# Optimization experiments

Measured on AMD Instinct MI355X. Metric: run time of the kernel, lower is better.

## Reference

```python
import jax, jax.numpy as jnp
import numpy as np

N_NODES = 100000
N_EDGES = 1600000
IN_DIM, H_DIM, OUT_DIM = 256, 128, 2
NEG_SLOPE = 0.2  # PyG GATConv default


def gat_conv(x, edge_index, W, a_src, a_dst, b):
    """Single-head PyG GATConv (heads=1, concat, add_self_loops=True)."""
    n = x.shape[0]
    loops = jnp.arange(n, dtype=edge_index.dtype)
    src = jnp.concatenate([edge_index[0], loops])  # [E+N]
    dst = jnp.concatenate([edge_index[1], loops])
    h = x @ W                                      # [N, F_out]
    # attention logits per edge: LeakyReLU(a_src.h_src + a_dst.h_dst)
    e = jax.nn.leaky_relu((h @ a_src)[src] + (h @ a_dst)[dst], NEG_SLOPE)
    # segment softmax over incoming edges of each destination node
    m = jax.ops.segment_max(e, dst, num_segments=n)
    ex = jnp.exp(e - m[dst])
    denom = jax.ops.segment_sum(ex, dst, num_segments=n)
    alpha = ex / denom[dst]                        # self-loops guarantee denom > 0
    # scatter-aggregate weighted messages
    out = jax.ops.segment_sum(h[src] * alpha[:, None], dst, num_segments=n)
    return out + b


def setup_inputs() -> dict:
    key = jax.random.key(0)
    ks = jax.random.split(key, 10)
    glorot = lambda k, shape: jax.random.normal(k, shape, dtype=jnp.float32) * jnp.sqrt(
        2.0 / (shape[0] + shape[-1])
    ).astype(jnp.float32)
    return {
        "x": jax.random.normal(ks[0], (N_NODES, IN_DIM), dtype=jnp.float32),
        "edge_index": jax.random.randint(ks[1], (2, N_EDGES), 0, N_NODES, dtype=jnp.int64 if jax.config.jax_enable_x64 else jnp.int32),
        "W1": glorot(ks[2], (IN_DIM, H_DIM)),
        "a1_src": glorot(ks[3], (H_DIM,)),
        "a1_dst": glorot(ks[4], (H_DIM,)),
        "b1": jnp.zeros((H_DIM,), dtype=jnp.float32),
        "W2": glorot(ks[5], (H_DIM, OUT_DIM)),
        "a2_src": glorot(ks[6], (OUT_DIM,)),
        "a2_dst": glorot(ks[7], (OUT_DIM,)),
        "b2": jnp.zeros((OUT_DIM,), dtype=jnp.float32),
    }


def reference(x, edge_index, W1, a1_src, a1_dst, b1, W2, a2_src, a2_dst, b2):
    h1 = jax.nn.relu(gat_conv(x, edge_index, W1, a1_src, a1_dst, b1))
    # F.dropout(p=0.5) is identity in eval mode
    return gat_conv(h1, edge_index, W2, a2_src, a2_dst, b2)
```

## Files before the change

### kernel.cpp

```cpp
#include <hip/hip_runtime.h>
#include <hip/hip_bf16.h>

#define N_NODES 100000
#define IN_DIM 256
#define H_DIM 128
#define NEG_SLOPE 0.2f

#define NBUCK 391
#define BKT_CAP 8192
#define P1_EPT 16

__device__ __forceinline__ float lrelu(float v) { return v > 0.f ? v : NEG_SLOPE * v; }
__device__ __forceinline__ float bflo(unsigned u) { return __uint_as_float(u << 16); }
__device__ __forceinline__ float bfhi(unsigned u) { return __uint_as_float(u & 0xffff0000u); }
__device__ __forceinline__ unsigned short f2bf(float f) {
    unsigned u = __float_as_uint(f);
    return (unsigned short)((u + 0x7fffu + ((u >> 16) & 1u)) >> 16);
}
__device__ __forceinline__ float rdlanef(float v, int j) {
    return __uint_as_float(__builtin_amdgcn_readlane(__float_as_uint(v), j));
}

typedef short bfrag __attribute__((ext_vector_type(8)));
typedef float f32x4 __attribute__((ext_vector_type(4)));

__global__ __launch_bounds__(512) void fused_gemm_bin1(const float* __restrict__ x,
                                                       const float* __restrict__ W,
                                                       const float* __restrict__ a_src,
                                                       const float* __restrict__ a_dst,
                                                       unsigned short* __restrict__ hb,
                                                       float* __restrict__ as1,
                                                       float* __restrict__ ad1,
                                                       const int* __restrict__ src,
                                                       const int* __restrict__ dst,
                                                       int* __restrict__ bktAlloc,
                                                       unsigned long long* __restrict__ tmp,
                                                       int E, int p1B) {
    __shared__ __align__(16) char smemraw[65536];
    const int tid = threadIdx.x;

    if ((int)blockIdx.x < p1B) {
        int* hist  = (int*)smemraw;
        int* basev = hist + 512;
        int* hist2 = basev + 512;
        hist[tid] = 0; hist2[tid] = 0;
        __syncthreads();
        const int e0 = blockIdx.x * (512 * P1_EPT) + tid * P1_EPT;
        int sv[P1_EPT], dv[P1_EPT];
#pragma unroll
        for (int i = 0; i < P1_EPT; ++i) {
            int e = e0 + i;
            if (e < E) { sv[i] = src[e]; dv[i] = dst[e]; }
            else dv[i] = -1;
        }
#pragma unroll
        for (int i = 0; i < P1_EPT; ++i)
            if (dv[i] >= 0) atomicAdd(&hist[dv[i] >> 8], 1);
        __syncthreads();
        {
            int c = hist[tid];
            basev[tid] = c ? atomicAdd(&bktAlloc[tid], c) : 0;
        }
        __syncthreads();
#pragma unroll
        for (int i = 0; i < P1_EPT; ++i) {
            if (dv[i] >= 0) {
                int b = dv[i] >> 8;
                int r = atomicAdd(&hist2[b], 1);
                int pos = basev[b] + r;
                if (pos < BKT_CAP)
                    tmp[(size_t)b * BKT_CAP + pos] =
                        ((unsigned long long)(unsigned)dv[i] << 32) | (unsigned)sv[i];
            }
        }
        return;
    }

    unsigned short* lds = (unsigned short*)smemraw;
    const int w = tid >> 6;
    const int lane = tid & 63;
    const int lo = lane & 15;
    const int hi = lane >> 4;
    const int row0 = ((int)blockIdx.x - p1B) * 128;

    {
        int col = tid & 127;
        int kb = tid >> 7;
        int c7 = col & 7;
#pragma unroll
        for (int i = 0; i < 16; ++i) {
            int k0 = i * 16 + kb * 4;
            float w0 = W[(k0 + 0) * H_DIM + col];
            float w1 = W[(k0 + 1) * H_DIM + col];
            float w2 = W[(k0 + 2) * H_DIM + col];
            float w3 = W[(k0 + 3) * H_DIM + col];
            int kblk = k0 >> 3;
            int rem = k0 & 7;
            unsigned short* d = &lds[col * 256 + ((kblk ^ c7) << 3) + rem];
            d[0] = f2bf(w0); d[1] = f2bf(w1); d[2] = f2bf(w2); d[3] = f2bf(w3);
        }
    }
    __syncthreads();

    int arow = row0 + w * 16 + lo;
    if (arow >= N_NODES) arow = N_NODES - 1;
    const float* xrow = x + (size_t)arow * IN_DIM + hi * 8;

    f32x4 acc[8] = {};
#pragma unroll
    for (int kc = 0; kc < 8; ++kc) {
        float4 xa = *reinterpret_cast<const float4*>(xrow + kc * 32);
        float4 xb = *reinterpret_cast<const float4*>(xrow + kc * 32 + 4);
        bfrag a;
        a[0] = (short)f2bf(xa.x); a[1] = (short)f2bf(xa.y);
        a[2] = (short)f2bf(xa.z); a[3] = (short)f2bf(xa.w);
        a[4] = (short)f2bf(xb.x); a[5] = (short)f2bf(xb.y);
        a[6] = (short)f2bf(xb.z); a[7] = (short)f2bf(xb.w);
        int kblk = kc * 4 + hi;
#pragma unroll
        for (int c = 0; c < 8; ++c) {
            int col = c * 16 + lo;
            const bfrag b = *reinterpret_cast<const bfrag*>(
                &lds[col * 256 + ((kblk ^ (col & 7)) << 3)]);
            acc[c] = __builtin_amdgcn_mfma_f32_16x16x32_bf16(a, b, acc[c], 0, 0, 0);
        }
    }

    float asv[8], adv[8];
#pragma unroll
    for (int c = 0; c < 8; ++c) { asv[c] = a_src[c * 16 + lo]; adv[c] = a_dst[c * 16 + lo]; }
#pragma unroll
    for (int q = 0; q < 4; ++q) {
        float ps = 0.f, pd = 0.f;
#pragma unroll
        for (int c = 0; c < 8; ++c) { ps += acc[c][q] * asv[c]; pd += acc[c][q] * adv[c]; }
#pragma unroll
        for (int off = 8; off; off >>= 1) {
            ps += __shfl_xor(ps, off);
            pd += __shfl_xor(pd, off);
        }
        int grow = row0 + w * 16 + hi * 4 + q;
        if (lo == 0 && grow < N_NODES) { as1[grow] = ps; ad1[grow] = pd; }
    }

    __syncthreads();
#pragma unroll
    for (int c = 0; c < 8; ++c)
#pragma unroll
        for (int q = 0; q < 4; ++q)
            lds[(w * 16 + hi * 4 + q) * 128 + c * 16 + lo] = f2bf(acc[c][q]);
    __syncthreads();
#pragma unroll
    for (int i = 0; i < 4; ++i) {
        int idx = i * 512 + tid;
        int row = idx >> 4;
        int chunk = idx & 15;
        int grow = row0 + row;
        if (grow < N_NODES) {
            uint4 v = *reinterpret_cast<const uint4*>(&lds[row * 128 + chunk * 8]);
            *reinterpret_cast<uint4*>(&hb[(size_t)grow * H_DIM + chunk * 8]) = v;
        }
    }
}

__global__ __launch_bounds__(512) void bin_pass2(const unsigned long long* __restrict__ tmp,
                                                 const int* __restrict__ bktAlloc,
                                                 int* __restrict__ rowptr,
                                                 int* __restrict__ col) {
    __shared__ int bscan[512];
    __shared__ int cnt[256], sc[256], rp[256];
    __shared__ int s_ebeg;
    const int b = blockIdx.x;
    const int nb0 = b << 8;
    const int nmax = min(256, N_NODES - nb0);
    const int tid = threadIdx.x;

    int v = (tid < NBUCK) ? min(bktAlloc[tid], BKT_CAP) : 0;
    bscan[tid] = v;
    __syncthreads();
    for (int off = 1; off < 512; off <<= 1) {
        int u = (tid >= off) ? bscan[tid - off] : 0;
        __syncthreads();
        bscan[tid] += u;
        __syncthreads();
    }
    const int myCnt = min(bktAlloc[b], BKT_CAP);
    if (tid == 0) s_ebeg = bscan[b] - myCnt;
    if (tid < 256) cnt[tid] = 0;
    __syncthreads();
    const int ebeg = s_ebeg;
    const unsigned long long* btmp = tmp + (size_t)b * BKT_CAP;

    for (int i = tid; i < myCnt; i += 512)
        atomicAdd(&cnt[(int)(unsigned)(btmp[i] >> 32) - nb0], 1);
    __syncthreads();
    if (tid < 256) sc[tid] = cnt[tid];
    __syncthreads();
    for (int off = 1; off < 256; off <<= 1) {
        int u = (tid < 256 && tid >= off) ? sc[tid - off] : 0;
        __syncthreads();
        if (tid < 256) sc[tid] += u;
        __syncthreads();
    }
    if (tid < 256) { rp[tid] = ebeg + sc[tid] - cnt[tid]; cnt[tid] = 0; }
    __syncthreads();
    if (tid < nmax) rowptr[nb0 + tid] = rp[tid];
    if (b == NBUCK - 1 && tid == 0) rowptr[N_NODES] = ebeg + myCnt;
    for (int i = tid; i < myCnt; i += 512) {
        unsigned long long e = btmp[i];
        int s = (int)(unsigned)e;
        int dl = (int)(unsigned)(e >> 32) - nb0;
        int off = atomicAdd(&cnt[dl], 1);
        col[rp[dl] + off] = s;
    }
}

__global__ __launch_bounds__(256) void agg1_kernel(const unsigned int* __restrict__ hbu,
                                                   const float* __restrict__ as1,
                                                   const float* __restrict__ ad1,
                                                   const int* __restrict__ rowptr,
                                                   const int* __restrict__ col,
                                                   const float* __restrict__ b1,
                                                   const float* __restrict__ W2,
                                                   const float* __restrict__ a2s,
                                                   const float* __restrict__ a2d,
                                                   float* __restrict__ h2,
                                                   float* __restrict__ as2,
                                                   float* __restrict__ ad2) {
    int node = blockIdx.x * 4 + (threadIdx.x >> 6);
    int lane = threadIdx.x & 63;
    if (node >= N_NODES) return;

    float adi = ad1[node];
    float wself = __expf(lrelu(as1[node] + adi));
    unsigned hvs = hbu[(unsigned)node * 64u + lane];
    float ax = wself * bflo(hvs), ay = wself * bfhi(hvs);
    float lsum = 0.0f;

    const int beg = rowptr[node], end = rowptr[node + 1];
    for (int p0 = beg; p0 < end; p0 += 64) {
        const int jn = min(64, end - p0);
        int idx = p0 + (lane < jn ? lane : 0);
        int s_l = col[idx];
        float e_l = (lane < jn) ? __expf(lrelu(as1[s_l] + adi)) : 0.0f;
        lsum += e_l;
        int j = 0;
        for (; j + 8 <= jn; j += 8) {
            const unsigned* r0 = hbu + ((size_t)__builtin_amdgcn_readlane(s_l, j)     << 6);
            const unsigned* r1 = hbu + ((size_t)__builtin_amdgcn_readlane(s_l, j + 1) << 6);
            const unsigned* r2 = hbu + ((size_t)__builtin_amdgcn_readlane(s_l, j + 2) << 6);
            const unsigned* r3 = hbu + ((size_t)__builtin_amdgcn_readlane(s_l, j + 3) << 6);
            const unsigned* r4 = hbu + ((size_t)__builtin_amdgcn_readlane(s_l, j + 4) << 6);
            const unsigned* r5 = hbu + ((size_t)__builtin_amdgcn_readlane(s_l, j + 5) << 6);
            const unsigned* r6 = hbu + ((size_t)__builtin_amdgcn_readlane(s_l, j + 6) << 6);
            const unsigned* r7 = hbu + ((size_t)__builtin_amdgcn_readlane(s_l, j + 7) << 6);
            unsigned v0 = r0[lane];
            unsigned v1 = r1[lane];
            unsigned v2 = r2[lane];
            unsigned v3 = r3[lane];
            unsigned v4 = r4[lane];
            unsigned v5 = r5[lane];
            unsigned v6 = r6[lane];
            unsigned v7 = r7[lane];
            float w0 = rdlanef(e_l, j);
            float w1 = rdlanef(e_l, j + 1);
            float w2 = rdlanef(e_l, j + 2);
            float w3 = rdlanef(e_l, j + 3);
            float w4 = rdlanef(e_l, j + 4);
            float w5 = rdlanef(e_l, j + 5);
            float w6 = rdlanef(e_l, j + 6);
            float w7 = rdlanef(e_l, j + 7);
            ax += (w0 * bflo(v0) + w1 * bflo(v1)) + (w2 * bflo(v2) + w3 * bflo(v3))
                + (w4 * bflo(v4) + w5 * bflo(v5)) + (w6 * bflo(v6) + w7 * bflo(v7));
            ay += (w0 * bfhi(v0) + w1 * bfhi(v1)) + (w2 * bfhi(v2) + w3 * bfhi(v3))
                + (w4 * bfhi(v4) + w5 * bfhi(v5)) + (w6 * bfhi(v6) + w7 * bfhi(v7));
        }
        for (; j < jn; ++j) {
            const unsigned* r = hbu + ((size_t)__builtin_amdgcn_readlane(s_l, j) << 6);
            float w = rdlanef(e_l, j);
            unsigned v = r[lane];
            ax += w * bflo(v);
            ay += w * bfhi(v);
        }
    }
#pragma unroll
    for (int off = 32; off; off >>= 1) lsum += __shfl_xor(lsum, off);
    float inv = 1.0f / (lsum + wself);

    float2 bb = *reinterpret_cast<const float2*>(&b1[lane * 2]);
    float o0 = fmaxf(ax * inv + bb.x, 0.0f);
    float o1 = fmaxf(ay * inv + bb.y, 0.0f);

    float4 w2 = *reinterpret_cast<const float4*>(&W2[lane * 4]);
    float p0 = o0 * w2.x + o1 * w2.z;
    float p1 = o0 * w2.y + o1 * w2.w;
#pragma unroll
    for (int off = 32; off; off >>= 1) {
        p0 += __shfl_xor(p0, off);
        p1 += __shfl_xor(p1, off);
    }
    if (lane == 0) {
        h2[node * 2 + 0] = p0;
        h2[node * 2 + 1] = p1;
        as2[node] = p0 * a2s[0] + p1 * a2s[1];
        ad2[node] = p0 * a2d[0] + p1 * a2d[1];
    }
}

__global__ __launch_bounds__(256) void agg2_kernel(const float* __restrict__ h2,
                                                   const float* __restrict__ as2,
                                                   const float* __restrict__ ad2,
                                                   const int* __restrict__ rowptr,
                                                   const int* __restrict__ col,
                                                   const float* __restrict__ b2,
                                                   float* __restrict__ out) {
    int node = blockIdx.x * 256 + threadIdx.x;
    if (node >= N_NODES) return;
    const float2* __restrict__ h2v = (const float2*)h2;
    float adi = ad2[node];
    float w0s = __expf(lrelu(as2[node] + adi));
    float l = w0s;
    float2 hv0 = h2v[(unsigned)node];
    float a0 = w0s * hv0.x, a1 = w0s * hv0.y;
    int p = rowptr[node], end = rowptr[node + 1];
    for (; p + 4 <= end; p += 4) {
        unsigned s0 = (unsigned)col[p],     s1 = (unsigned)col[p + 1];
        unsigned s2 = (unsigned)col[p + 2], s3 = (unsigned)col[p + 3];
        float w0 = __expf(lrelu(as2[s0] + adi));
        float w1 = __expf(lrelu(as2[s1] + adi));
        float w2 = __expf(lrelu(as2[s2] + adi));
        float w3 = __expf(lrelu(as2[s3] + adi));
        float2 v0 = h2v[s0];
        float2 v1 = h2v[s1];
        float2 v2 = h2v[s2];
        float2 v3 = h2v[s3];
        l += (w0 + w1) + (w2 + w3);
        a0 += (w0 * v0.x + w1 * v1.x) + (w2 * v2.x + w3 * v3.x);
        a1 += (w0 * v0.y + w1 * v1.y) + (w2 * v2.y + w3 * v3.y);
    }
    for (; p < end; ++p) {
        unsigned s = (unsigned)col[p];
        float w = __expf(lrelu(as2[s] + adi));
        float2 hv = h2v[s];
        l += w;
        a0 += w * hv.x;
        a1 += w * hv.y;
    }
    float inv = 1.0f / l;
    out[node * 2 + 0] = a0 * inv + b2[0];
    out[node * 2 + 1] = a1 * inv + b2[1];
}

static inline char* ws_bump(char*& p, size_t bytes) {
    char* r = p;
    p += (bytes + 255) & ~(size_t)255;
    return r;
}

extern "C" void kernel_launch(void* const* d_in, const int* in_sizes, int n_in,
                              void* d_out, int out_size, void* d_ws, size_t ws_size,
                              hipStream_t stream) {
    const float* x   = (const float*)d_in[0];
    const int*   ei  = (const int*)d_in[1];
    const float* W1  = (const float*)d_in[2];
    const float* a1s = (const float*)d_in[3];
    const float* a1d = (const float*)d_in[4];
    const float* b1  = (const float*)d_in[5];
    const float* W2  = (const float*)d_in[6];
    const float* a2s = (const float*)d_in[7];
    const float* a2d = (const float*)d_in[8];
    const float* b2  = (const float*)d_in[9];
    float* out = (float*)d_out;

    const int E = in_sizes[1] / 2;
    const int* src = ei;
    const int* dstp = ei + E;

    char* p = (char*)d_ws;
    unsigned short* hb = (unsigned short*)ws_bump(p, (size_t)N_NODES * H_DIM * 2);
    unsigned long long* tmp = (unsigned long long*)ws_bump(p, (size_t)NBUCK * BKT_CAP * 8);
    float* as1    = (float*)ws_bump(p, (size_t)N_NODES * 4);
    float* ad1    = (float*)ws_bump(p, (size_t)N_NODES * 4);
    int*   rowptr = (int*)  ws_bump(p, (size_t)(N_NODES + 1) * 4);
    int*   col    = (int*)  ws_bump(p, (size_t)E * 4);
    int*   bktAlloc = (int*)ws_bump(p, 512 * 4);
    float* h2     = (float*)ws_bump(p, (size_t)N_NODES * 2 * 4);
    float* as2    = (float*)ws_bump(p, (size_t)N_NODES * 4);
    float* ad2    = (float*)ws_bump(p, (size_t)N_NODES * 4);

    const int nodeBlocks = (N_NODES + 255) / 256;
    const int p1Blocks = (E + 512 * P1_EPT - 1) / (512 * P1_EPT);
    const int gemmBlocks = (N_NODES + 127) / 128;

    hipMemsetAsync(bktAlloc, 0, 512 * 4, stream);

    fused_gemm_bin1<<<p1Blocks + gemmBlocks, 512, 0, stream>>>(
        x, W1, a1s, a1d, hb, as1, ad1, src, dstp, bktAlloc, tmp, E, p1Blocks);
    bin_pass2<<<NBUCK, 512, 0, stream>>>(tmp, bktAlloc, rowptr, col);

    agg1_kernel<<<(N_NODES + 3) / 4, 256, 0, stream>>>((const unsigned int*)hb, as1, ad1,
                                                       rowptr, col, b1, W2, a2s, a2d,
                                                       h2, as2, ad2);
    agg2_kernel<<<nodeBlocks, 256, 0, stream>>>(h2, as2, ad2, rowptr, col, b2, out);
}
```

Before: 155.4 us.

## Pack bin entries to 32-bit, double GEMM row tile, widen bin pass

Edge bin entries are packed into 32-bit words holding a 17-bit source and an 8-bit local destination, instead of 64-bit pairs. This halves the scratch traffic between the two binning passes. The GEMM part now gives each block 256 rows as two accumulator panels sharing the same LDS-resident W fragments, and bin_pass2 runs with 1024 threads. The added launch_bounds occupancy hint together with the doubled accumulators may push register pressure high enough to cause spills.

```diff
diff --git a/kernel.cpp b/kernel.cpp
--- a/kernel.cpp
+++ b/kernel.cpp
@@ -24,7 +24,7 @@
 typedef short bfrag __attribute__((ext_vector_type(8)));
 typedef float f32x4 __attribute__((ext_vector_type(4)));
 
-__global__ __launch_bounds__(512) void fused_gemm_bin1(const float* __restrict__ x,
+__global__ __launch_bounds__(512, 4) void fused_gemm_bin1(const float* __restrict__ x,
                                                        const float* __restrict__ W,
                                                        const float* __restrict__ a_src,
                                                        const float* __restrict__ a_dst,
@@ -34,7 +34,7 @@
                                                        const int* __restrict__ src,
                                                        const int* __restrict__ dst,
                                                        int* __restrict__ bktAlloc,
-                                                       unsigned long long* __restrict__ tmp,
+                                                       unsigned* __restrict__ tmp,
                                                        int E, int p1B) {
     __shared__ __align__(16) char smemraw[65536];
     const int tid = threadIdx.x;
@@ -69,8 +69,8 @@
                 int r = atomicAdd(&hist2[b], 1);
                 int pos = basev[b] + r;
                 if (pos < BKT_CAP)
-                    tmp[(size_t)b * BKT_CAP + pos] =
-                        ((unsigned long long)(unsigned)dv[i] << 32) | (unsigned)sv[i];
+                    tmp[b * BKT_CAP + pos] =
+                        ((unsigned)(dv[i] & 255) << 17) | (unsigned)sv[i];
             }
         }
         return;
@@ -81,7 +81,7 @@
     const int lane = tid & 63;
     const int lo = lane & 15;
     const int hi = lane >> 4;
-    const int row0 = ((int)blockIdx.x - p1B) * 128;
+    const int row0 = ((int)blockIdx.x - p1B) * 256;
 
     {
         int col = tid & 127;
@@ -102,27 +102,37 @@
     }
     __syncthreads();
 
-    int arow = row0 + w * 16 + lo;
-    if (arow >= N_NODES) arow = N_NODES - 1;
-    const float* xrow = x + (size_t)arow * IN_DIM + hi * 8;
-
-    f32x4 acc[8] = {};
+    int arow0 = row0 + w * 16 + lo;
+    int arow1 = arow0 + 128;
+    if (arow0 >= N_NODES) arow0 = N_NODES - 1;
+    if (arow1 >= N_NODES) arow1 = N_NODES - 1;
+    const float* xr0 = x + (size_t)arow0 * IN_DIM + hi * 8;
+    const float* xr1 = x + (size_t)arow1 * IN_DIM + hi * 8;
+
+    f32x4 acc0[8] = {}, acc1[8] = {};
 #pragma unroll
     for (int kc = 0; kc < 8; ++kc) {
-        float4 xa = *reinterpret_cast<const float4*>(xrow + kc * 32);
-        float4 xb = *reinterpret_cast<const float4*>(xrow + kc * 32 + 4);
-        bfrag a;
-        a[0] = (short)f2bf(xa.x); a[1] = (short)f2bf(xa.y);
-        a[2] = (short)f2bf(xa.z); a[3] = (short)f2bf(xa.w);
-        a[4] = (short)f2bf(xb.x); a[5] = (short)f2bf(xb.y);
-        a[6] = (short)f2bf(xb.z); a[7] = (short)f2bf(xb.w);
+        float4 xa0 = *reinterpret_cast<const float4*>(xr0 + kc * 32);
+        float4 xb0 = *reinterpret_cast<const float4*>(xr0 + kc * 32 + 4);
+        float4 xa1 = *reinterpret_cast<const float4*>(xr1 + kc * 32);
+        float4 xb1 = *reinterpret_cast<const float4*>(xr1 + kc * 32 + 4);
+        bfrag a0, a1;
+        a0[0] = (short)f2bf(xa0.x); a0[1] = (short)f2bf(xa0.y);
+        a0[2] = (short)f2bf(xa0.z); a0[3] = (short)f2bf(xa0.w);
+        a0[4] = (short)f2bf(xb0.x); a0[5] = (short)f2bf(xb0.y);
+        a0[6] = (short)f2bf(xb0.z); a0[7] = (short)f2bf(xb0.w);
+        a1[0] = (short)f2bf(xa1.x); a1[1] = (short)f2bf(xa1.y);
+        a1[2] = (short)f2bf(xa1.z); a1[3] = (short)f2bf(xa1.w);
+        a1[4] = (short)f2bf(xb1.x); a1[5] = (short)f2bf(xb1.y);
+        a1[6] = (short)f2bf(xb1.z); a1[7] = (short)f2bf(xb1.w);
         int kblk = kc * 4 + hi;
 #pragma unroll
         for (int c = 0; c < 8; ++c) {
             int col = c * 16 + lo;
             const bfrag b = *reinterpret_cast<const bfrag*>(
                 &lds[col * 256 + ((kblk ^ (col & 7)) << 3)]);
-            acc[c] = __builtin_amdgcn_mfma_f32_16x16x32_bf16(a, b, acc[c], 0, 0, 0);
+            acc0[c] = __builtin_amdgcn_mfma_f32_16x16x32_bf16(a0, b, acc0[c], 0, 0, 0);
+            acc1[c] = __builtin_amdgcn_mfma_f32_16x16x32_bf16(a1, b, acc1[c], 0, 0, 0);
         }
     }
 
@@ -130,28 +140,34 @@
 #pragma unroll
     for (int c = 0; c < 8; ++c) { asv[c] = a_src[c * 16 + lo]; adv[c] = a_dst[c * 16 + lo]; }
 #pragma unroll
-    for (int q = 0; q < 4; ++q) {
-        float ps = 0.f, pd = 0.f;
-#pragma unroll
-        for (int c = 0; c < 8; ++c) { ps += acc[c][q] * asv[c]; pd += acc[c][q] * adv[c]; }
-#pragma unroll
-        for (int off = 8; off; off >>= 1) {
-            ps += __shfl_xor(ps, off);
-            pd += __shfl_xor(pd, off);
-        }
-        int grow = row0 + w * 16 + hi * 4 + q;
-        if (lo == 0 && grow < N_NODES) { as1[grow] = ps; ad1[grow] = pd; }
+    for (int pnl = 0; pnl < 2; ++pnl) {
+        const f32x4* acc = pnl ? acc1 : acc0;
+#pragma unroll
+        for (int q = 0; q < 4; ++q) {
+            float ps = 0.f, pd = 0.f;
+#pragma unroll
+            for (int c = 0; c < 8; ++c) { ps += acc[c][q] * asv[c]; pd += acc[c][q] * adv[c]; }
+#pragma unroll
+            for (int off = 8; off; off >>= 1) {
+                ps += __shfl_xor(ps, off);
+                pd += __shfl_xor(pd, off);
+            }
+            int grow = row0 + pnl * 128 + w * 16 + hi * 4 + q;
+            if (lo == 0 && grow < N_NODES) { as1[grow] = ps; ad1[grow] = pd; }
+        }
     }
 
     __syncthreads();
 #pragma unroll
     for (int c = 0; c < 8; ++c)
 #pragma unroll
-        for (int q = 0; q < 4; ++q)
-            lds[(w * 16 + hi * 4 + q) * 128 + c * 16 + lo] = f2bf(acc[c][q]);
-    __syncthreads();
-#pragma unroll
-    for (int i = 0; i < 4; ++i) {
+        for (int q = 0; q < 4; ++q) {
+            lds[(w * 16 + hi * 4 + q) * 128 + c * 16 + lo] = f2bf(acc0[c][q]);
+            lds[(128 + w * 16 + hi * 4 + q) * 128 + c * 16 + lo] = f2bf(acc1[c][q]);
+        }
+    __syncthreads();
+#pragma unroll
+    for (int i = 0; i < 8; ++i) {
         int idx = i * 512 + tid;
         int row = idx >> 4;
         int chunk = idx & 15;
@@ -163,11 +179,11 @@
     }
 }
 
-__global__ __launch_bounds__(512) void bin_pass2(const unsigned long long* __restrict__ tmp,
-                                                 const int* __restrict__ bktAlloc,
-                                                 int* __restrict__ rowptr,
-                                                 int* __restrict__ col) {
-    __shared__ int bscan[512];
+__global__ __launch_bounds__(1024) void bin_pass2(const unsigned* __restrict__ tmp,
+                                                  const int* __restrict__ bktAlloc,
+                                                  int* __restrict__ rowptr,
+                                                  int* __restrict__ col) {
+    __shared__ int bscan[1024];
     __shared__ int cnt[256], sc[256], rp[256];
     __shared__ int s_ebeg;
     const int b = blockIdx.x;
@@ -189,10 +205,10 @@
     if (tid < 256) cnt[tid] = 0;
     __syncthreads();
     const int ebeg = s_ebeg;
-    const unsigned long long* btmp = tmp + (size_t)b * BKT_CAP;
-
-    for (int i = tid; i < myCnt; i += 512)
-        atomicAdd(&cnt[(int)(unsigned)(btmp[i] >> 32) - nb0], 1);
+    const unsigned* btmp = tmp + (size_t)b * BKT_CAP;
+
+    for (int i = tid; i < myCnt; i += 1024)
+        atomicAdd(&cnt[btmp[i] >> 17], 1);
     __syncthreads();
     if (tid < 256) sc[tid] = cnt[tid];
     __syncthreads();
@@ -206,10 +222,10 @@
     __syncthreads();
     if (tid < nmax) rowptr[nb0 + tid] = rp[tid];
     if (b == NBUCK - 1 && tid == 0) rowptr[N_NODES] = ebeg + myCnt;
-    for (int i = tid; i < myCnt; i += 512) {
-        unsigned long long e = btmp[i];
-        int s = (int)(unsigned)e;
-        int dl = (int)(unsigned)(e >> 32) - nb0;
+    for (int i = tid; i < myCnt; i += 1024) {
+        unsigned e = btmp[i];
+        int s = (int)(e & 0x1FFFFu);
+        int dl = (int)(e >> 17);
         int off = atomicAdd(&cnt[dl], 1);
         col[rp[dl] + off] = s;
     }
@@ -378,7 +394,7 @@
 
     char* p = (char*)d_ws;
     unsigned short* hb = (unsigned short*)ws_bump(p, (size_t)N_NODES * H_DIM * 2);
-    unsigned long long* tmp = (unsigned long long*)ws_bump(p, (size_t)NBUCK * BKT_CAP * 8);
+    unsigned* tmp = (unsigned*)ws_bump(p, (size_t)NBUCK * BKT_CAP * 4);
     float* as1    = (float*)ws_bump(p, (size_t)N_NODES * 4);
     float* ad1    = (float*)ws_bump(p, (size_t)N_NODES * 4);
     int*   rowptr = (int*)  ws_bump(p, (size_t)(N_NODES + 1) * 4);
@@ -390,13 +406,13 @@
 
     const int nodeBlocks = (N_NODES + 255) / 256;
     const int p1Blocks = (E + 512 * P1_EPT - 1) / (512 * P1_EPT);
-    const int gemmBlocks = (N_NODES + 127) / 128;
+    const int gemmBlocks = (N_NODES + 255) / 256;
 
     hipMemsetAsync(bktAlloc, 0, 512 * 4, stream);
 
     fused_gemm_bin1<<<p1Blocks + gemmBlocks, 512, 0, stream>>>(
         x, W1, a1s, a1d, hb, as1, ad1, src, dstp, bktAlloc, tmp, E, p1Blocks);
-    bin_pass2<<<NBUCK, 512, 0, stream>>>(tmp, bktAlloc, rowptr, col);
+    bin_pass2<<<NBUCK, 1024, 0, stream>>>(tmp, bktAlloc, rowptr, col);
 
     agg1_kernel<<<(N_NODES + 3) / 4, 256, 0, stream>>>((const unsigned int*)hb, as1, ad1,
                                                        rowptr, col, b1, W2, a2s, a2d,
```

Result: no change. 154.2 us (-0.8%).

## Fuse CSR build into layer-1 aggregation with per-bucket LDS sort

Applied to the files above, without the earlier changes.

The second binning pass is folded into agg1. Each block now owns a 128-node bucket, counting-sorts that bucket's edges in LDS and aggregates directly from the LDS column list. It also writes a per-bucket column array and packed (offset, degree) node info for agg2. Edge records shrink from 64-bit to packed 32-bit words and bucket count doubles. This removes one kernel launch, the global bucket-size scan and rowptr. The cost is only 782 agg1 blocks of 8 waves, which lowers parallelism, plus an 8-bit degree field and a 17-bit source field that assume bounded degree and node count.

```diff
diff --git a/kernel.cpp b/kernel.cpp
--- a/kernel.cpp
+++ b/kernel.cpp
@@ -6,8 +6,8 @@
 #define H_DIM 128
 #define NEG_SLOPE 0.2f
 
-#define NBUCK 391
-#define BKT_CAP 8192
+#define NBUCK 782
+#define BKT_CAP 4096
 #define P1_EPT 16
 
 __device__ __forceinline__ float lrelu(float v) { return v > 0.f ? v : NEG_SLOPE * v; }
@@ -34,16 +34,17 @@
                                                        const int* __restrict__ src,
                                                        const int* __restrict__ dst,
                                                        int* __restrict__ bktAlloc,
-                                                       unsigned long long* __restrict__ tmp,
+                                                       unsigned* __restrict__ tmp,
                                                        int E, int p1B) {
     __shared__ __align__(16) char smemraw[65536];
     const int tid = threadIdx.x;
 
     if ((int)blockIdx.x < p1B) {
         int* hist  = (int*)smemraw;
-        int* basev = hist + 512;
-        int* hist2 = basev + 512;
-        hist[tid] = 0; hist2[tid] = 0;
+        int* basev = hist + 1024;
+        int* hist2 = basev + 1024;
+        hist[tid] = 0; hist[tid + 512] = 0;
+        hist2[tid] = 0; hist2[tid + 512] = 0;
         __syncthreads();
         const int e0 = blockIdx.x * (512 * P1_EPT) + tid * P1_EPT;
         int sv[P1_EPT], dv[P1_EPT];
@@ -55,22 +56,22 @@
         }
 #pragma unroll
         for (int i = 0; i < P1_EPT; ++i)
-            if (dv[i] >= 0) atomicAdd(&hist[dv[i] >> 8], 1);
-        __syncthreads();
-        {
-            int c = hist[tid];
-            basev[tid] = c ? atomicAdd(&bktAlloc[tid], c) : 0;
+            if (dv[i] >= 0) atomicAdd(&hist[dv[i] >> 7], 1);
+        __syncthreads();
+        for (int t = tid; t < NBUCK; t += 512) {
+            int c = hist[t];
+            basev[t] = c ? atomicAdd(&bktAlloc[t], c) : 0;
         }
         __syncthreads();
 #pragma unroll
         for (int i = 0; i < P1_EPT; ++i) {
             if (dv[i] >= 0) {
-                int b = dv[i] >> 8;
+                int b = dv[i] >> 7;
                 int r = atomicAdd(&hist2[b], 1);
                 int pos = basev[b] + r;
                 if (pos < BKT_CAP)
-                    tmp[(size_t)b * BKT_CAP + pos] =
-                        ((unsigned long long)(unsigned)dv[i] << 32) | (unsigned)sv[i];
+                    tmp[b * BKT_CAP + pos] =
+                        ((unsigned)(dv[i] & 127) << 17) | (unsigned)sv[i];
             }
         }
         return;
@@ -163,169 +164,147 @@
     }
 }
 
-__global__ __launch_bounds__(512) void bin_pass2(const unsigned long long* __restrict__ tmp,
-                                                 const int* __restrict__ bktAlloc,
-                                                 int* __restrict__ rowptr,
-                                                 int* __restrict__ col) {
-    __shared__ int bscan[512];
-    __shared__ int cnt[256], sc[256], rp[256];
-    __shared__ int s_ebeg;
-    const int b = blockIdx.x;
-    const int nb0 = b << 8;
-    const int nmax = min(256, N_NODES - nb0);
-    const int tid = threadIdx.x;
-
-    int v = (tid < NBUCK) ? min(bktAlloc[tid], BKT_CAP) : 0;
-    bscan[tid] = v;
-    __syncthreads();
-    for (int off = 1; off < 512; off <<= 1) {
-        int u = (tid >= off) ? bscan[tid - off] : 0;
-        __syncthreads();
-        bscan[tid] += u;
-        __syncthreads();
-    }
-    const int myCnt = min(bktAlloc[b], BKT_CAP);
-    if (tid == 0) s_ebeg = bscan[b] - myCnt;
-    if (tid < 256) cnt[tid] = 0;
-    __syncthreads();
-    const int ebeg = s_ebeg;
-    const unsigned long long* btmp = tmp + (size_t)b * BKT_CAP;
-
-    for (int i = tid; i < myCnt; i += 512)
-        atomicAdd(&cnt[(int)(unsigned)(btmp[i] >> 32) - nb0], 1);
-    __syncthreads();
-    if (tid < 256) sc[tid] = cnt[tid];
-    __syncthreads();
-    for (int off = 1; off < 256; off <<= 1) {
-        int u = (tid < 256 && tid >= off) ? sc[tid - off] : 0;
-        __syncthreads();
-        if (tid < 256) sc[tid] += u;
-        __syncthreads();
-    }
-    if (tid < 256) { rp[tid] = ebeg + sc[tid] - cnt[tid]; cnt[tid] = 0; }
-    __syncthreads();
-    if (tid < nmax) rowptr[nb0 + tid] = rp[tid];
-    if (b == NBUCK - 1 && tid == 0) rowptr[N_NODES] = ebeg + myCnt;
-    for (int i = tid; i < myCnt; i += 512) {
-        unsigned long long e = btmp[i];
-        int s = (int)(unsigned)e;
-        int dl = (int)(unsigned)(e >> 32) - nb0;
-        int off = atomicAdd(&cnt[dl], 1);
-        col[rp[dl] + off] = s;
-    }
-}
-
-__global__ __launch_bounds__(256) void agg1_kernel(const unsigned int* __restrict__ hbu,
+__global__ __launch_bounds__(512) void agg1_kernel(const unsigned int* __restrict__ hbu,
                                                    const float* __restrict__ as1,
                                                    const float* __restrict__ ad1,
-                                                   const int* __restrict__ rowptr,
-                                                   const int* __restrict__ col,
+                                                   const unsigned* __restrict__ tmp,
+                                                   const int* __restrict__ bktAlloc,
                                                    const float* __restrict__ b1,
                                                    const float* __restrict__ W2,
                                                    const float* __restrict__ a2s,
                                                    const float* __restrict__ a2d,
                                                    float* __restrict__ h2,
                                                    float* __restrict__ as2,
-                                                   float* __restrict__ ad2) {
-    int node = blockIdx.x * 4 + (threadIdx.x >> 6);
-    int lane = threadIdx.x & 63;
-    if (node >= N_NODES) return;
-
-    float adi = ad1[node];
-    float wself = __expf(lrelu(as1[node] + adi));
-    unsigned hvs = hbu[(unsigned)node * 64u + lane];
-    float ax = wself * bflo(hvs), ay = wself * bfhi(hvs);
-    float lsum = 0.0f;
-
-    const int beg = rowptr[node], end = rowptr[node + 1];
-    for (int p0 = beg; p0 < end; p0 += 64) {
-        const int jn = min(64, end - p0);
-        int idx = p0 + (lane < jn ? lane : 0);
-        int s_l = col[idx];
-        float e_l = (lane < jn) ? __expf(lrelu(as1[s_l] + adi)) : 0.0f;
-        lsum += e_l;
-        int j = 0;
-        for (; j + 8 <= jn; j += 8) {
-            const unsigned* r0 = hbu + ((size_t)__builtin_amdgcn_readlane(s_l, j)     << 6);
-            const unsigned* r1 = hbu + ((size_t)__builtin_amdgcn_readlane(s_l, j + 1) << 6);
-            const unsigned* r2 = hbu + ((size_t)__builtin_amdgcn_readlane(s_l, j + 2) << 6);
-            const unsigned* r3 = hbu + ((size_t)__builtin_amdgcn_readlane(s_l, j + 3) << 6);
-            const unsigned* r4 = hbu + ((size_t)__builtin_amdgcn_readlane(s_l, j + 4) << 6);
-            const unsigned* r5 = hbu + ((size_t)__builtin_amdgcn_readlane(s_l, j + 5) << 6);
-            const unsigned* r6 = hbu + ((size_t)__builtin_amdgcn_readlane(s_l, j + 6) << 6);
-            const unsigned* r7 = hbu + ((size_t)__builtin_amdgcn_readlane(s_l, j + 7) << 6);
-            unsigned v0 = r0[lane];
-            unsigned v1 = r1[lane];
-            unsigned v2 = r2[lane];
-            unsigned v3 = r3[lane];
-            unsigned v4 = r4[lane];
-            unsigned v5 = r5[lane];
-            unsigned v6 = r6[lane];
-            unsigned v7 = r7[lane];
-            float w0 = rdlanef(e_l, j);
-            float w1 = rdlanef(e_l, j + 1);
-            float w2 = rdlanef(e_l, j + 2);
-            float w3 = rdlanef(e_l, j + 3);
-            float w4 = rdlanef(e_l, j + 4);
-            float w5 = rdlanef(e_l, j + 5);
-            float w6 = rdlanef(e_l, j + 6);
-            float w7 = rdlanef(e_l, j + 7);
-            ax += (w0 * bflo(v0) + w1 * bflo(v1)) + (w2 * bflo(v2) + w3 * bflo(v3))
-                + (w4 * bflo(v4) + w5 * bflo(v5)) + (w6 * bflo(v6) + w7 * bflo(v7));
-            ay += (w0 * bfhi(v0) + w1 * bfhi(v1)) + (w2 * bfhi(v2) + w3 * bfhi(v3))
-                + (w4 * bfhi(v4) + w5 * bfhi(v5)) + (w6 * bfhi(v6) + w7 * bfhi(v7));
-        }
-        for (; j < jn; ++j) {
-            const unsigned* r = hbu + ((size_t)__builtin_amdgcn_readlane(s_l, j) << 6);
-            float w = rdlanef(e_l, j);
-            unsigned v = r[lane];
-            ax += w * bflo(v);
-            ay += w * bfhi(v);
-        }
-    }
-#pragma unroll
-    for (int off = 32; off; off >>= 1) lsum += __shfl_xor(lsum, off);
-    float inv = 1.0f / (lsum + wself);
-
+                                                   float* __restrict__ ad2,
+                                                   unsigned* __restrict__ colG,
+                                                   unsigned* __restrict__ nodeInfo) {
+    __shared__ unsigned raw[BKT_CAP];
+    __shared__ unsigned colL[BKT_CAP];
+    __shared__ int cnt_s[128], sc_s[128], rp_s[128];
+    const int b = blockIdx.x;
+    const int nb0 = b << 7;
+    const int tid = threadIdx.x;
+    const int myCnt = min(bktAlloc[b], BKT_CAP);
+
+    if (tid < 128) cnt_s[tid] = 0;
+    __syncthreads();
+    for (int i = tid; i < myCnt; i += 512) {
+        unsigned e = tmp[b * BKT_CAP + i];
+        raw[i] = e;
+        atomicAdd(&cnt_s[e >> 17], 1);
+    }
+    __syncthreads();
+    if (tid < 128) sc_s[tid] = cnt_s[tid];
+    __syncthreads();
+    for (int off = 1; off < 128; off <<= 1) {
+        int u = (tid < 128 && tid >= off) ? sc_s[tid - off] : 0;
+        __syncthreads();
+        if (tid < 128) sc_s[tid] += u;
+        __syncthreads();
+    }
+    if (tid < 128) { rp_s[tid] = sc_s[tid] - cnt_s[tid]; cnt_s[tid] = 0; }
+    __syncthreads();
+    for (int i = tid; i < myCnt; i += 512) {
+        unsigned e = raw[i];
+        int dl = e >> 17;
+        int o = atomicAdd(&cnt_s[dl], 1);
+        colL[rp_s[dl] + o] = e & 0x1FFFFu;
+    }
+    __syncthreads();
+    for (int i = tid; i < myCnt; i += 512) colG[b * BKT_CAP + i] = colL[i];
+    if (tid < 128 && nb0 + tid < N_NODES)
+        nodeInfo[nb0 + tid] = ((unsigned)rp_s[tid] << 8) | (unsigned)cnt_s[tid];
+
+    const int wv = tid >> 6;
+    const int lane = tid & 63;
     float2 bb = *reinterpret_cast<const float2*>(&b1[lane * 2]);
-    float o0 = fmaxf(ax * inv + bb.x, 0.0f);
-    float o1 = fmaxf(ay * inv + bb.y, 0.0f);
-
     float4 w2 = *reinterpret_cast<const float4*>(&W2[lane * 4]);
-    float p0 = o0 * w2.x + o1 * w2.z;
-    float p1 = o0 * w2.y + o1 * w2.w;
-#pragma unroll
-    for (int off = 32; off; off >>= 1) {
-        p0 += __shfl_xor(p0, off);
-        p1 += __shfl_xor(p1, off);
-    }
-    if (lane == 0) {
-        h2[node * 2 + 0] = p0;
-        h2[node * 2 + 1] = p1;
-        as2[node] = p0 * a2s[0] + p1 * a2s[1];
-        ad2[node] = p0 * a2d[0] + p1 * a2d[1];
+    float a2s0 = a2s[0], a2s1 = a2s[1], a2d0 = a2d[0], a2d1 = a2d[1];
+
+    for (int ni = wv; ni < 128; ni += 8) {
+        int node = nb0 + ni;
+        if (node >= N_NODES) break;
+        const int beg = rp_s[ni], deg = cnt_s[ni];
+        float adi = ad1[node];
+        float wself = __expf(lrelu(as1[node] + adi));
+        unsigned hvs = hbu[(unsigned)node * 64u + lane];
+        float ax = wself * bflo(hvs), ay = wself * bfhi(hvs);
+        float lsum = 0.0f;
+
+        for (int p0 = 0; p0 < deg; p0 += 64) {
+            const int jn = min(64, deg - p0);
+            int s_l = (int)colL[beg + p0 + (lane < jn ? lane : 0)];
+            float e_l = (lane < jn) ? __expf(lrelu(as1[s_l] + adi)) : 0.0f;
+            lsum += e_l;
+            int j = 0;
+            for (; j + 4 <= jn; j += 4) {
+                const unsigned* r0 = hbu + ((size_t)__builtin_amdgcn_readlane(s_l, j)     << 6);
+                const unsigned* r1 = hbu + ((size_t)__builtin_amdgcn_readlane(s_l, j + 1) << 6);
+                const unsigned* r2 = hbu + ((size_t)__builtin_amdgcn_readlane(s_l, j + 2) << 6);
+                const unsigned* r3 = hbu + ((size_t)__builtin_amdgcn_readlane(s_l, j + 3) << 6);
+                unsigned v0 = r0[lane];
+                unsigned v1 = r1[lane];
+                unsigned v2 = r2[lane];
+                unsigned v3 = r3[lane];
+                float w0 = rdlanef(e_l, j);
+                float w1 = rdlanef(e_l, j + 1);
+                float w2f = rdlanef(e_l, j + 2);
+                float w3 = rdlanef(e_l, j + 3);
+                ax += (w0 * bflo(v0) + w1 * bflo(v1)) + (w2f * bflo(v2) + w3 * bflo(v3));
+                ay += (w0 * bfhi(v0) + w1 * bfhi(v1)) + (w2f * bfhi(v2) + w3 * bfhi(v3));
+            }
+            for (; j < jn; ++j) {
+                const unsigned* r = hbu + ((size_t)__builtin_amdgcn_readlane(s_l, j) << 6);
+                float w = rdlanef(e_l, j);
+                unsigned v = r[lane];
+                ax += w * bflo(v);
+                ay += w * bfhi(v);
+            }
+        }
+#pragma unroll
+        for (int off = 32; off; off >>= 1) lsum += __shfl_xor(lsum, off);
+        float inv = 1.0f / (lsum + wself);
+
+        float o0 = fmaxf(ax * inv + bb.x, 0.0f);
+        float o1 = fmaxf(ay * inv + bb.y, 0.0f);
+
+        float p0 = o0 * w2.x + o1 * w2.z;
+        float p1 = o0 * w2.y + o1 * w2.w;
+#pragma unroll
+        for (int off = 32; off; off >>= 1) {
+            p0 += __shfl_xor(p0, off);
+            p1 += __shfl_xor(p1, off);
+        }
+        if (lane == 0) {
+            h2[node * 2 + 0] = p0;
+            h2[node * 2 + 1] = p1;
+            as2[node] = p0 * a2s0 + p1 * a2s1;
+            ad2[node] = p0 * a2d0 + p1 * a2d1;
+        }
     }
 }
 
 __global__ __launch_bounds__(256) void agg2_kernel(const float* __restrict__ h2,
                                                    const float* __restrict__ as2,
                                                    const float* __restrict__ ad2,
-                                                   const int* __restrict__ rowptr,
-                                                   const int* __restrict__ col,
+                                                   const unsigned* __restrict__ colG,
+                                                   const unsigned* __restrict__ nodeInfo,
                                                    const float* __restrict__ b2,
                                                    float* __restrict__ out) {
     int node = blockIdx.x * 256 + threadIdx.x;
     if (node >= N_NODES) return;
     const float2* __restrict__ h2v = (const float2*)h2;
+    unsigned info = nodeInfo[node];
+    const unsigned* cp = colG + (size_t)(node >> 7) * BKT_CAP + (info >> 8);
+    const int deg = (int)(info & 255u);
     float adi = ad2[node];
     float w0s = __expf(lrelu(as2[node] + adi));
     float l = w0s;
     float2 hv0 = h2v[(unsigned)node];
     float a0 = w0s * hv0.x, a1 = w0s * hv0.y;
-    int p = rowptr[node], end = rowptr[node + 1];
-    for (; p + 4 <= end; p += 4) {
-        unsigned s0 = (unsigned)col[p],     s1 = (unsigned)col[p + 1];
-        unsigned s2 = (unsigned)col[p + 2], s3 = (unsigned)col[p + 3];
+    int p = 0;
+    for (; p + 4 <= deg; p += 4) {
+        unsigned s0 = cp[p], s1 = cp[p + 1], s2 = cp[p + 2], s3 = cp[p + 3];
         float w0 = __expf(lrelu(as2[s0] + adi));
         float w1 = __expf(lrelu(as2[s1] + adi));
         float w2 = __expf(lrelu(as2[s2] + adi));
@@ -338,8 +317,8 @@
         a0 += (w0 * v0.x + w1 * v1.x) + (w2 * v2.x + w3 * v3.x);
         a1 += (w0 * v0.y + w1 * v1.y) + (w2 * v2.y + w3 * v3.y);
     }
-    for (; p < end; ++p) {
-        unsigned s = (unsigned)col[p];
+    for (; p < deg; ++p) {
+        unsigned s = cp[p];
         float w = __expf(lrelu(as2[s] + adi));
         float2 hv = h2v[s];
         l += w;
@@ -378,12 +357,12 @@
 
     char* p = (char*)d_ws;
     unsigned short* hb = (unsigned short*)ws_bump(p, (size_t)N_NODES * H_DIM * 2);
-    unsigned long long* tmp = (unsigned long long*)ws_bump(p, (size_t)NBUCK * BKT_CAP * 8);
+    unsigned* tmp  = (unsigned*)ws_bump(p, (size_t)NBUCK * BKT_CAP * 4);
+    unsigned* colG = (unsigned*)ws_bump(p, (size_t)NBUCK * BKT_CAP * 4);
+    unsigned* nodeInfo = (unsigned*)ws_bump(p, (size_t)N_NODES * 4);
     float* as1    = (float*)ws_bump(p, (size_t)N_NODES * 4);
     float* ad1    = (float*)ws_bump(p, (size_t)N_NODES * 4);
-    int*   rowptr = (int*)  ws_bump(p, (size_t)(N_NODES + 1) * 4);
-    int*   col    = (int*)  ws_bump(p, (size_t)E * 4);
-    int*   bktAlloc = (int*)ws_bump(p, 512 * 4);
+    int*   bktAlloc = (int*)ws_bump(p, 1024 * 4);
     float* h2     = (float*)ws_bump(p, (size_t)N_NODES * 2 * 4);
     float* as2    = (float*)ws_bump(p, (size_t)N_NODES * 4);
     float* ad2    = (float*)ws_bump(p, (size_t)N_NODES * 4);
@@ -392,14 +371,13 @@
     const int p1Blocks = (E + 512 * P1_EPT - 1) / (512 * P1_EPT);
     const int gemmBlocks = (N_NODES + 127) / 128;
 
-    hipMemsetAsync(bktAlloc, 0, 512 * 4, stream);
+    hipMemsetAsync(bktAlloc, 0, 1024 * 4, stream);
 
     fused_gemm_bin1<<<p1Blocks + gemmBlocks, 512, 0, stream>>>(
         x, W1, a1s, a1d, hb, as1, ad1, src, dstp, bktAlloc, tmp, E, p1Blocks);
-    bin_pass2<<<NBUCK, 512, 0, stream>>>(tmp, bktAlloc, rowptr, col);
-
-    agg1_kernel<<<(N_NODES + 3) / 4, 256, 0, stream>>>((const unsigned int*)hb, as1, ad1,
-                                                       rowptr, col, b1, W2, a2s, a2d,
-                                                       h2, as2, ad2);
-    agg2_kernel<<<nodeBlocks, 256, 0, stream>>>(h2, as2, ad2, rowptr, col, b2, out);
-}
+
+    agg1_kernel<<<NBUCK, 512, 0, stream>>>((const unsigned int*)hb, as1, ad1,
+                                           tmp, bktAlloc, b1, W2, a2s, a2d,
+                                           h2, as2, ad2, colG, nodeInfo);
+    agg2_kernel<<<nodeBlocks, 256, 0, stream>>>(h2, as2, ad2, colG, nodeInfo, b2, out);
+}
```

Result: faster. 151.8 us (-2.3%).

## Pre-convert W to bf16 once and pack binned edges into 32-bit words

Applied to the files above, without the earlier changes.

A small new kernel converts W1 to transposed bf16 once, so each GEMM block reads B fragments straight from global/L2 and no longer fills a 64KB LDS tile. That drops the per-block LDS staging and sync and halves shared memory, which can raise occupancy. Edge binning now uses 782 buckets of 128 nodes, and each edge is packed as a 7-bit local dst plus 17-bit src in 32 bits instead of 64, halving temp traffic. bin_pass2 runs with 1024 threads. The risks are an extra launch, global reads in the MFMA inner loop in place of LDS, and smaller bucket capacity (4096) that could overflow on skewed graphs.

```diff
diff --git a/kernel.cpp b/kernel.cpp
--- a/kernel.cpp
+++ b/kernel.cpp
@@ -6,8 +6,8 @@
 #define H_DIM 128
 #define NEG_SLOPE 0.2f
 
-#define NBUCK 391
-#define BKT_CAP 8192
+#define NBUCK 782
+#define BKT_CAP 4096
 #define P1_EPT 16
 
 __device__ __forceinline__ float lrelu(float v) { return v > 0.f ? v : NEG_SLOPE * v; }
@@ -24,8 +24,19 @@
 typedef short bfrag __attribute__((ext_vector_type(8)));
 typedef float f32x4 __attribute__((ext_vector_type(4)));
 
+__global__ __launch_bounds__(256) void prep_w(const float* __restrict__ W,
+                                              unsigned short* __restrict__ Wb) {
+    int idx = blockIdx.x * 1024 + threadIdx.x;
+#pragma unroll
+    for (int it = 0; it < 4; ++it, idx += 256) {
+        int k = idx >> 7;
+        int col = idx & 127;
+        Wb[col * 256 + k] = f2bf(W[idx]);
+    }
+}
+
 __global__ __launch_bounds__(512) void fused_gemm_bin1(const float* __restrict__ x,
-                                                       const float* __restrict__ W,
+                                                       const unsigned short* __restrict__ Wb,
                                                        const float* __restrict__ a_src,
                                                        const float* __restrict__ a_dst,
                                                        unsigned short* __restrict__ hb,
@@ -34,16 +45,17 @@
                                                        const int* __restrict__ src,
                                                        const int* __restrict__ dst,
                                                        int* __restrict__ bktAlloc,
-                                                       unsigned long long* __restrict__ tmp,
+                                                       unsigned* __restrict__ tmp,
                                                        int E, int p1B) {
-    __shared__ __align__(16) char smemraw[65536];
+    __shared__ __align__(16) char smemraw[32768];
     const int tid = threadIdx.x;
 
     if ((int)blockIdx.x < p1B) {
         int* hist  = (int*)smemraw;
-        int* basev = hist + 512;
-        int* hist2 = basev + 512;
-        hist[tid] = 0; hist2[tid] = 0;
+        int* basev = hist + 1024;
+        int* hist2 = basev + 1024;
+        hist[tid] = 0; hist[tid + 512] = 0;
+        hist2[tid] = 0; hist2[tid + 512] = 0;
         __syncthreads();
         const int e0 = blockIdx.x * (512 * P1_EPT) + tid * P1_EPT;
         int sv[P1_EPT], dv[P1_EPT];
@@ -55,22 +67,22 @@
         }
 #pragma unroll
         for (int i = 0; i < P1_EPT; ++i)
-            if (dv[i] >= 0) atomicAdd(&hist[dv[i] >> 8], 1);
-        __syncthreads();
-        {
-            int c = hist[tid];
-            basev[tid] = c ? atomicAdd(&bktAlloc[tid], c) : 0;
+            if (dv[i] >= 0) atomicAdd(&hist[dv[i] >> 7], 1);
+        __syncthreads();
+        for (int t = tid; t < NBUCK; t += 512) {
+            int c = hist[t];
+            basev[t] = c ? atomicAdd(&bktAlloc[t], c) : 0;
         }
         __syncthreads();
 #pragma unroll
         for (int i = 0; i < P1_EPT; ++i) {
             if (dv[i] >= 0) {
-                int b = dv[i] >> 8;
+                int b = dv[i] >> 7;
                 int r = atomicAdd(&hist2[b], 1);
                 int pos = basev[b] + r;
                 if (pos < BKT_CAP)
-                    tmp[(size_t)b * BKT_CAP + pos] =
-                        ((unsigned long long)(unsigned)dv[i] << 32) | (unsigned)sv[i];
+                    tmp[b * BKT_CAP + pos] =
+                        ((unsigned)(dv[i] & 127) << 17) | (unsigned)sv[i];
             }
         }
         return;
@@ -83,28 +95,14 @@
     const int hi = lane >> 4;
     const int row0 = ((int)blockIdx.x - p1B) * 128;
 
-    {
-        int col = tid & 127;
-        int kb = tid >> 7;
-        int c7 = col & 7;
-#pragma unroll
-        for (int i = 0; i < 16; ++i) {
-            int k0 = i * 16 + kb * 4;
-            float w0 = W[(k0 + 0) * H_DIM + col];
-            float w1 = W[(k0 + 1) * H_DIM + col];
-            float w2 = W[(k0 + 2) * H_DIM + col];
-            float w3 = W[(k0 + 3) * H_DIM + col];
-            int kblk = k0 >> 3;
-            int rem = k0 & 7;
-            unsigned short* d = &lds[col * 256 + ((kblk ^ c7) << 3) + rem];
-            d[0] = f2bf(w0); d[1] = f2bf(w1); d[2] = f2bf(w2); d[3] = f2bf(w3);
-        }
-    }
-    __syncthreads();
-
     int arow = row0 + w * 16 + lo;
     if (arow >= N_NODES) arow = N_NODES - 1;
     const float* xrow = x + (size_t)arow * IN_DIM + hi * 8;
+
+    const unsigned short* wp[8];
+#pragma unroll
+    for (int c = 0; c < 8; ++c)
+        wp[c] = Wb + (size_t)((c * 16 + lo) * 256 + hi * 8);
 
     f32x4 acc[8] = {};
 #pragma unroll
@@ -116,12 +114,9 @@
         a[2] = (short)f2bf(xa.z); a[3] = (short)f2bf(xa.w);
         a[4] = (short)f2bf(xb.x); a[5] = (short)f2bf(xb.y);
         a[6] = (short)f2bf(xb.z); a[7] = (short)f2bf(xb.w);
-        int kblk = kc * 4 + hi;
 #pragma unroll
         for (int c = 0; c < 8; ++c) {
-            int col = c * 16 + lo;
-            const bfrag b = *reinterpret_cast<const bfrag*>(
-                &lds[col * 256 + ((kblk ^ (col & 7)) << 3)]);
+            const bfrag b = *reinterpret_cast<const bfrag*>(wp[c] + kc * 32);
             acc[c] = __builtin_amdgcn_mfma_f32_16x16x32_bf16(a, b, acc[c], 0, 0, 0);
         }
     }
@@ -163,22 +158,22 @@
     }
 }
 
-__global__ __launch_bounds__(512) void bin_pass2(const unsigned long long* __restrict__ tmp,
-                                                 const int* __restrict__ bktAlloc,
-                                                 int* __restrict__ rowptr,
-                                                 int* __restrict__ col) {
-    __shared__ int bscan[512];
-    __shared__ int cnt[256], sc[256], rp[256];
+__global__ __launch_bounds__(1024) void bin_pass2(const unsigned* __restrict__ tmp,
+                                                  const int* __restrict__ bktAlloc,
+                                                  int* __restrict__ rowptr,
+                                                  int* __restrict__ col) {
+    __shared__ int bscan[1024];
+    __shared__ int cnt[128], sc[128], rp[128];
     __shared__ int s_ebeg;
     const int b = blockIdx.x;
-    const int nb0 = b << 8;
-    const int nmax = min(256, N_NODES - nb0);
+    const int nb0 = b << 7;
+    const int nmax = min(128, N_NODES - nb0);
     const int tid = threadIdx.x;
 
     int v = (tid < NBUCK) ? min(bktAlloc[tid], BKT_CAP) : 0;
     bscan[tid] = v;
     __syncthreads();
-    for (int off = 1; off < 512; off <<= 1) {
+    for (int off = 1; off < 1024; off <<= 1) {
         int u = (tid >= off) ? bscan[tid - off] : 0;
         __syncthreads();
         bscan[tid] += u;
@@ -186,30 +181,30 @@
     }
     const int myCnt = min(bktAlloc[b], BKT_CAP);
     if (tid == 0) s_ebeg = bscan[b] - myCnt;
-    if (tid < 256) cnt[tid] = 0;
+    if (tid < 128) cnt[tid] = 0;
     __syncthreads();
     const int ebeg = s_ebeg;
-    const unsigned long long* btmp = tmp + (size_t)b * BKT_CAP;
-
-    for (int i = tid; i < myCnt; i += 512)
-        atomicAdd(&cnt[(int)(unsigned)(btmp[i] >> 32) - nb0], 1);
-    __syncthreads();
-    if (tid < 256) sc[tid] = cnt[tid];
-    __syncthreads();
-    for (int off = 1; off < 256; off <<= 1) {
-        int u = (tid < 256 && tid >= off) ? sc[tid - off] : 0;
-        __syncthreads();
-        if (tid < 256) sc[tid] += u;
-        __syncthreads();
-    }
-    if (tid < 256) { rp[tid] = ebeg + sc[tid] - cnt[tid]; cnt[tid] = 0; }
+    const unsigned* btmp = tmp + (size_t)b * BKT_CAP;
+
+    for (int i = tid; i < myCnt; i += 1024)
+        atomicAdd(&cnt[btmp[i] >> 17], 1);
+    __syncthreads();
+    if (tid < 128) sc[tid] = cnt[tid];
+    __syncthreads();
+    for (int off = 1; off < 128; off <<= 1) {
+        int u = (tid < 128 && tid >= off) ? sc[tid - off] : 0;
+        __syncthreads();
+        if (tid < 128) sc[tid] += u;
+        __syncthreads();
+    }
+    if (tid < 128) { rp[tid] = ebeg + sc[tid] - cnt[tid]; cnt[tid] = 0; }
     __syncthreads();
     if (tid < nmax) rowptr[nb0 + tid] = rp[tid];
     if (b == NBUCK - 1 && tid == 0) rowptr[N_NODES] = ebeg + myCnt;
-    for (int i = tid; i < myCnt; i += 512) {
-        unsigned long long e = btmp[i];
-        int s = (int)(unsigned)e;
-        int dl = (int)(unsigned)(e >> 32) - nb0;
+    for (int i = tid; i < myCnt; i += 1024) {
+        unsigned e = btmp[i];
+        int s = (int)(e & 0x1FFFFu);
+        int dl = (int)(e >> 17);
         int off = atomicAdd(&cnt[dl], 1);
         col[rp[dl] + off] = s;
     }
@@ -378,12 +373,13 @@
 
     char* p = (char*)d_ws;
     unsigned short* hb = (unsigned short*)ws_bump(p, (size_t)N_NODES * H_DIM * 2);
-    unsigned long long* tmp = (unsigned long long*)ws_bump(p, (size_t)NBUCK * BKT_CAP * 8);
+    unsigned* tmp  = (unsigned*)ws_bump(p, (size_t)NBUCK * BKT_CAP * 4);
+    unsigned short* Wb = (unsigned short*)ws_bump(p, (size_t)IN_DIM * H_DIM * 2);
     float* as1    = (float*)ws_bump(p, (size_t)N_NODES * 4);
     float* ad1    = (float*)ws_bump(p, (size_t)N_NODES * 4);
     int*   rowptr = (int*)  ws_bump(p, (size_t)(N_NODES + 1) * 4);
     int*   col    = (int*)  ws_bump(p, (size_t)E * 4);
-    int*   bktAlloc = (int*)ws_bump(p, 512 * 4);
+    int*   bktAlloc = (int*)ws_bump(p, 1024 * 4);
     float* h2     = (float*)ws_bump(p, (size_t)N_NODES * 2 * 4);
     float* as2    = (float*)ws_bump(p, (size_t)N_NODES * 4);
     float* ad2    = (float*)ws_bump(p, (size_t)N_NODES * 4);
@@ -392,11 +388,12 @@
     const int p1Blocks = (E + 512 * P1_EPT - 1) / (512 * P1_EPT);
     const int gemmBlocks = (N_NODES + 127) / 128;
 
-    hipMemsetAsync(bktAlloc, 0, 512 * 4, stream);
+    hipMemsetAsync(bktAlloc, 0, 1024 * 4, stream);
+    prep_w<<<32, 256, 0, stream>>>(W1, Wb);
 
     fused_gemm_bin1<<<p1Blocks + gemmBlocks, 512, 0, stream>>>(
-        x, W1, a1s, a1d, hb, as1, ad1, src, dstp, bktAlloc, tmp, E, p1Blocks);
-    bin_pass2<<<NBUCK, 512, 0, stream>>>(tmp, bktAlloc, rowptr, col);
+        x, Wb, a1s, a1d, hb, as1, ad1, src, dstp, bktAlloc, tmp, E, p1Blocks);
+    bin_pass2<<<NBUCK, 1024, 0, stream>>>(tmp, bktAlloc, rowptr, col);
 
     agg1_kernel<<<(N_NODES + 3) / 4, 256, 0, stream>>>((const unsigned int*)hb, as1, ad1,
                                                        rowptr, col, b1, W2, a2s, a2d,
```

After: 194.0 us. 24.8% more time.
